# Optimization experiments

Hardware: AMD Instinct MI355X
Metric: run time of the kernel (lower is better)

Reference implementation:

```python
import jax, jax.numpy as jnp
import numpy as np

T, N = 20, 192
D_EMB, D_H, D_REL = 32, 64, 32
D_TMP = D_REL + 2 * D_H  # 160 = rel_emb + h_self + h_neighbor


def setup_inputs() -> dict:
    key = jax.random.key(0)
    ks = jax.random.split(key, 16)
    g = lambda i, shape, s: jax.random.normal(ks[i], shape, jnp.float32) * s
    inp = {
        "nodes_abs": g(0, (T, N, 2), 1.0),
        "nodes_norm": g(1, (T, N, 2), 1.0),
        "shift_value": g(2, (T, N, 2), 1.0),
        # parameters (inputLayer, LSTMCell, 2 GCNs, outputLayer)
        "w_in": g(3, (D_EMB, 2), 0.2),
        "b_in": jnp.zeros((D_EMB,), jnp.float32),
        "w_ih": g(4, (4 * D_H, D_EMB), 0.1),
        "w_hh": g(5, (4 * D_H, D_H), 0.001),
        "b_ih": jnp.zeros((4 * D_H,), jnp.float32).at[D_H:2 * D_H].set(1.0),
        "b_hh": jnp.zeros((4 * D_H,), jnp.float32),
        "w_rel": g(6, (2, D_REL, 2), 0.1),
        "b_rel": jnp.zeros((2, D_REL), jnp.float32),
        "w_gate": g(7, (2, D_H, D_TMP), 0.1),
        "b_gate": jnp.zeros((2, D_H), jnp.float32),
        "w_ar": g(8, (2, D_TMP), 0.1),
        "b_ar": jnp.zeros((2,), jnp.float32),
        "w_nei": g(9, (2, D_H, D_H), 0.1),
        "w_out": g(10, (2, D_H), 0.1),
        "b_out": jnp.zeros((2,), jnp.float32),
        # int inputs
        "seq_list": jax.random.randint(ks[11], (T, N), 0, 2).astype(jnp.int32),
        "nei_list": jax.random.randint(ks[12], (T, N, N), 0, 2).astype(jnp.int32),
        "nei_num": jax.random.randint(ks[13], (T, N), 0, N).astype(jnp.int32),
    }
    return inp


def reference(nodes_abs, nodes_norm, shift_value, w_in, b_in, w_ih, w_hh, b_ih, b_hh,
              w_rel, b_rel, w_gate, b_gate, w_ar, b_ar, w_nei, w_out, b_out,
              seq_list, nei_list, nei_num):
    eps = 1e-6

    def gcn(p, corr, nei_f, h, c, o):
        # corr: (N,N,2) relative positions pos_i - pos_j; nei_f: (N,N) 0/1 mask
        r = jax.nn.relu(jnp.einsum('ijd,rd->ijr', corr, w_rel[p]) + b_rel[p])
        tmp = jnp.concatenate([r,
                               jnp.broadcast_to(h[:, None, :], (N, N, D_H)),
                               jnp.broadcast_to(h[None, :, :], (N, N, D_H))], axis=-1)
        gate = jax.nn.sigmoid(jnp.einsum('ijt,ht->ijh', tmp, w_gate[p]) + b_gate[p])
        score = jnp.einsum('ijt,t->ij', tmp, w_ar[p]) + b_ar[p]
        score = jnp.where(nei_f > 0, score, -1e9)
        pos = jax.nn.softmax(score, axis=1) * nei_f  # masked attention over neighbors j
        msg = jnp.einsum('ij,ijh,jh->ih', pos, gate, h)  # gated, attended aggregation
        c_new = c + msg @ w_nei[p].T
        h_new = o * jnp.tanh(c_new)
        v1 = jnp.sum(gate * nei_f[:, :, None]) / (jnp.sum(nei_f) * D_H + eps)
        v2 = jnp.sum(jnp.max(pos, axis=1)) / (jnp.sum(jnp.max(nei_f, axis=1)) + eps)
        v3 = jnp.sum(nei_f) / jnp.float32(N)
        return h_new, c_new, (v1, v2, v3)

    def step(carry, xs):
        h, c, v1s, v2s, v3s = carry
        abs_t, norm_t, seq_t, nei_t = xs
        m = seq_t > 0
        mf = m.astype(jnp.float32)
        nei_f = (nei_t > 0).astype(jnp.float32) * mf[:, None] * mf[None, :]
        corr = abs_t[:, None, :] - abs_t[None, :, :]  # corr_index[i,j] = pos_i - pos_j
        x = jax.nn.relu(norm_t @ w_in.T + b_in)  # dropout is identity in eval
        gates = x @ w_ih.T + b_ih + h @ w_hh.T + b_hh
        i_g, f_g, g_g, o_g = jnp.split(gates, 4, axis=-1)
        i_g = jax.nn.sigmoid(i_g); f_g = jax.nn.sigmoid(f_g); o_g = jax.nn.sigmoid(o_g)
        c1 = f_g * c + i_g * jnp.tanh(g_g)
        h1 = o_g * jnp.tanh(c1)
        h1, c1, look = gcn(0, corr, nei_f, h1, c1, o_g)
        h1, c1, _ = gcn(1, corr, nei_f, h1, c1, o_g)
        out_t = (h1 @ w_out.T + b_out) * mf[:, None]
        h = jnp.where(m[:, None], h1, h)  # only active nodes update state
        c = jnp.where(m[:, None], c1, c)
        return (h, c, v1s + look[0], v2s + look[1], v3s + look[2]), out_t

    h0 = jnp.zeros((N, D_H), jnp.float32)
    c0 = jnp.zeros((N, D_H), jnp.float32)
    z = jnp.float32(0.0)
    xs = (nodes_abs[:-1], nodes_norm[:-1], seq_list[:-1], nei_list[:-1])
    (h, c, v1, v2, v3), outs = jax.lax.scan(step, (h0, c0, z, z, z), xs)
    outputs = jnp.concatenate([outs, jnp.zeros((1, N, 2), jnp.float32)], axis=0)
    return outputs, h, c, (v1 / T, v2 / T, v3 / T)
```

## Files before the change

### kernel.cpp

```cpp
#include <hip/hip_runtime.h>
#include <hip/hip_bf16.h>

#define T_STEPS 20
#define NSTEP   19
#define NN      192
#define DH      64
#define DE      32

enum : int {
  O_H     = 0,
  O_C     = O_H    + NN*DH,
  O_UH0   = O_C    + NN*DH,
  O_UH1   = O_UH0  + 2*NN*DH,
  O_CW    = O_UH1  + 2*NN*DH,
  O_OG    = O_CW   + NN*DH,
  O_U1    = O_OG   + NN*DH,
  O_S1    = O_U1   + NN*DH,
  O_S20   = O_S1   + NN,
  O_S21   = O_S20  + NN,
  O_ACC   = O_S21  + NN,
  O_WIHT  = O_ACC  + NSTEP*4 + 4,
  O_WHHT  = O_WIHT + 8192,
  O_BIH   = O_WHHT + 16384,
  O_WIN   = O_BIH  + 256,
  O_BIN   = O_WIN  + 64,
  O_WRELF = O_BIN  + 32,
  O_BRELF = O_WRELF+ 128,
  O_WGR   = O_BRELF+ 64,
  O_WGH1T = O_WGR  + 4096,
  O_WGH2T = O_WGH1T+ 8192,
  O_BGATE = O_WGH2T+ 8192,
  O_WARR  = O_BGATE+ 128,
  O_WARH1 = O_WARR + 64,
  O_WARH2 = O_WARH1+ 128,
  O_BAR   = O_WARH2+ 128,
  O_WNEIT = O_BAR  + 4,
  O_WOUT  = O_WNEIT+ 8192,
  O_BOUT  = O_WOUT + 128,
  O_ISF   = O_BOUT + 2,
  O_TOTAL = O_ISF  + 1
};

typedef unsigned long long ull;

__device__ __forceinline__ float bf2f(__hip_bfloat16 v) { return __bfloat162float(v); }
__device__ __forceinline__ float sigm(float x) { return 1.0f / (1.0f + __expf(-x)); }
__device__ __forceinline__ float tanh_fast(float x) {
  float e = __expf(-2.0f * fabsf(x));
  float r = (1.0f - e) / (1.0f + e);
  return copysignf(r, x);
}

__device__ __forceinline__ float ldf(const void* p, int idx, int isf32) {
  if (isf32) return ((const float*)p)[idx];
  return bf2f(((const __hip_bfloat16*)p)[idx]);
}
__device__ __forceinline__ void stf(void* p, int idx, float v, int isf32) {
  if (isf32) ((float*)p)[idx] = v;
  else       ((__hip_bfloat16*)p)[idx] = __float2bfloat16(v);
}

__device__ __forceinline__ int read_isf(const float* F, int tid, int* s_isf) {
  if (tid == 0) *s_isf = (int)F[O_ISF];
  __syncthreads();
  return *s_isf;
}

__device__ __forceinline__ void lstm_prep_dev(
    float* __restrict__ F, const void* __restrict__ nnorm, int isf32,
    int t, int i, int tid, int wave, int lane, int load_hc,
    float* s_x, float* s_hc, float* s_cc, float* s_gates, float* s_h1)
{
  if (load_hc && wave == 0) { s_hc[lane] = F[O_H + i*DH + lane]; s_cc[lane] = F[O_C + i*DH + lane]; }
  if (wave == 1 && lane < DE) {
    float nx = ldf(nnorm, (t*NN + i)*2 + 0, isf32);
    float ny = ldf(nnorm, (t*NN + i)*2 + 1, isf32);
    s_x[lane] = fmaxf(nx*F[O_WIN + lane*2] + ny*F[O_WIN + lane*2 + 1] + F[O_BIN + lane], 0.f);
  }
  __syncthreads();
  {
    int G = tid;
    float acc = F[O_BIH + G];
    for (int e = 0; e < DE; e++) acc += F[O_WIHT + e*256 + G] * s_x[e];
    for (int k = 0; k < DH; k++) acc += F[O_WHHT + k*256 + G] * s_hc[k];
    s_gates[G] = acc;
  }
  __syncthreads();
  if (wave == 0) {
    float ig = sigm(s_gates[lane]);
    float fg = sigm(s_gates[64 + lane]);
    float gg = tanh_fast(s_gates[128 + lane]);
    float og = sigm(s_gates[192 + lane]);
    float c1 = fg * s_cc[lane] + ig * gg;
    float h1 = og * tanh_fast(c1);
    int idx = i*DH + lane;
    F[O_CW  + idx] = c1;
    F[O_UH0 + 2*idx + 1] = h1;
    F[O_OG  + idx] = og;
    s_h1[lane] = h1;
  }
  __syncthreads();
  {
    int idx = i*DH + lane;
    if (wave == 0) {
      float a = 0.f;
      const float* w = F + O_WGH1T + lane;
      for (int k = 0; k < DH; k++) a += w[k*DH] * s_h1[k];
      F[O_U1 + idx] = a;
    } else if (wave == 1) {
      float a = 0.f;
      const float* w = F + O_WGH2T + lane;
      for (int k = 0; k < DH; k++) a += w[k*DH] * s_h1[k];
      F[O_UH0 + 2*idx] = a;
    } else if (wave == 2) {
      float hp = s_h1[lane];
      float a1 = hp * F[O_WARH1 + lane];
      float a2 = hp * F[O_WARH2 + lane];
      for (int o = 32; o >= 1; o >>= 1) { a1 += __shfl_xor(a1, o, 64); a2 += __shfl_xor(a2, o, 64); }
      if (lane == 0) { F[O_S1 + i] = a1; F[O_S20 + i] = a2; }
    }
  }
}

__global__ __launch_bounds__(256) void k_init(float* __restrict__ F,
                       void* __restrict__ out,
                       const void* w_in,  const void* b_in,
                       const void* w_ih,  const void* w_hh,
                       const void* b_ih,  const void* b_hh,
                       const void* w_rel, const void* b_rel,
                       const void* w_gate,const void* b_gate,
                       const void* w_ar,  const void* b_ar,
                       const void* w_nei, const void* w_out,
                       const void* b_out) {
  __shared__ int s_isf;
  const int wave = threadIdx.x >> 6, lane = threadIdx.x & 63;
  if (wave == 0) {
    const unsigned short* u = (const unsigned short*)w_gate;
    int bad = 0;
    for (int x = lane; x < 1024; x += 64) {
      float v = __uint_as_float(((unsigned)u[x]) << 16);
      if (!(fabsf(v) <= 4.0f)) bad++;
    }
    for (int o = 32; o >= 1; o >>= 1) bad += __shfl_xor(bad, o, 64);
    if (lane == 0) s_isf = (bad > 64);
  }
  __syncthreads();
  const int isf32 = s_isf;
  if (blockIdx.x == 0 && threadIdx.x == 0) F[O_ISF] = (float)isf32;

  int tid = blockIdx.x * blockDim.x + threadIdx.x;
  int stride = gridDim.x * blockDim.x;
  for (int x = tid; x < O_WIHT; x += stride) F[x] = 0.f;
  for (int x = tid; x < NN*2;  x += stride) stf(out, (T_STEPS-1)*NN*2 + x, 0.f, isf32);
  for (int x = tid; x < 8192;  x += stride) { int e = x >> 8, G = x & 255; F[O_WIHT + x] = ldf(w_ih, G*32 + e, isf32); }
  for (int x = tid; x < 16384; x += stride) { int k = x >> 8, G = x & 255; F[O_WHHT + x] = ldf(w_hh, G*64 + k, isf32); }
  for (int x = tid; x < 256;   x += stride) F[O_BIH + x] = ldf(b_ih, x, isf32) + ldf(b_hh, x, isf32);
  for (int x = tid; x < 64;    x += stride) F[O_WIN + x] = ldf(w_in, x, isf32);
  for (int x = tid; x < 32;    x += stride) F[O_BIN + x] = ldf(b_in, x, isf32);
  for (int x = tid; x < 128;   x += stride) F[O_WRELF + x] = ldf(w_rel, x, isf32);
  for (int x = tid; x < 64;    x += stride) F[O_BRELF + x] = ldf(b_rel, x, isf32);
  for (int x = tid; x < 4096;  x += stride) { int p = x >> 11, h = (x >> 5) & 63, d = x & 31;
    F[O_WGR + x] = ldf(w_gate, p*10240 + h*160 + d, isf32); }
  for (int x = tid; x < 8192;  x += stride) { int p = x >> 12, k = (x >> 6) & 63, h = x & 63;
    F[O_WGH1T + x] = ldf(w_gate, p*10240 + h*160 + 32 + k, isf32); }
  for (int x = tid; x < 8192;  x += stride) { int p = x >> 12, k = (x >> 6) & 63, h = x & 63;
    F[O_WGH2T + x] = ldf(w_gate, p*10240 + h*160 + 96 + k, isf32); }
  for (int x = tid; x < 128;   x += stride) F[O_BGATE + x] = ldf(b_gate, x, isf32);
  for (int x = tid; x < 64;    x += stride) { int p = x >> 5, d = x & 31; F[O_WARR + x] = ldf(w_ar, p*160 + d, isf32); }
  for (int x = tid; x < 128;   x += stride) { int p = x >> 6, k = x & 63; F[O_WARH1 + x] = ldf(w_ar, p*160 + 32 + k, isf32); }
  for (int x = tid; x < 128;   x += stride) { int p = x >> 6, k = x & 63; F[O_WARH2 + x] = ldf(w_ar, p*160 + 96 + k, isf32); }
  for (int x = tid; x < 2;     x += stride) F[O_BAR + x] = ldf(b_ar, x, isf32);
  for (int x = tid; x < 8192;  x += stride) { int p = x >> 12, k = (x >> 6) & 63, h = x & 63;
    F[O_WNEIT + x] = ldf(w_nei, p*4096 + h*64 + k, isf32); }
  for (int x = tid; x < 128;   x += stride) F[O_WOUT + x] = ldf(w_out, x, isf32);
  for (int x = tid; x < 2;     x += stride) F[O_BOUT + x] = ldf(b_out, x, isf32);
}

__global__ __launch_bounds__(256) void k_lstm0(float* __restrict__ F,
                                               const void* __restrict__ nnorm) {
  __shared__ float s_x[DE], s_hc[DH], s_cc[DH], s_gates[4*DH], s_h1[DH];
  __shared__ int s_isf;
  const int tid = threadIdx.x, wave = tid >> 6, lane = tid & 63;
  const int isf32 = read_isf(F, tid, &s_isf);
  lstm_prep_dev(F, nnorm, isf32, 0, blockIdx.x, tid, wave, lane, 1,
                s_x, s_hc, s_cc, s_gates, s_h1);
}

__global__ __launch_bounds__(256) void k_gcn(float* __restrict__ F,
                                             const void* __restrict__ nabs,
                                             const void* __restrict__ nnorm,
                                             const int* __restrict__ seq,
                                             const int* __restrict__ nei,
                                             void* __restrict__ out,
                                             int t, int p, int last) {
  __shared__ float s_rt[NN*33];
  __shared__ float s_score[NN], s_pos[NN], s_neif[NN];
  __shared__ int   s_jlist[NN];
  __shared__ float s_red[4*DH], s_v1[4], s_msg[DH], s_hprep[DH];
  __shared__ float s_x[DE], s_hc[DH], s_cc[DH], s_gates[4*DH], s_h1[DH];
  __shared__ int   s_isf, s_nv;

  const int tid = threadIdx.x, wave = tid >> 6, lane = tid & 63;
  const int i = blockIdx.x;
  const int isf32 = read_isf(F, tid, &s_isf);
  const int m_i = seq[t*NN + i] > 0;
  const int UHr = p ? O_UH1 : O_UH0;
  const int S2r = p ? O_S21 : O_S20;

  if (wave < 3) {
    int j  = wave*64 + lane;
    int nf = m_i && (seq[t*NN + j] > 0) && (nei[(t*NN + i)*NN + j] > 0);
    s_neif[j] = nf ? 1.f : 0.f;
    float sc = 0.f;
    if (nf) {
      float cx = ldf(nabs, (t*NN + i)*2 + 0, isf32) - ldf(nabs, (t*NN + j)*2 + 0, isf32);
      float cy = ldf(nabs, (t*NN + i)*2 + 1, isf32) - ldf(nabs, (t*NN + j)*2 + 1, isf32);
      const float* wr = F + O_WRELF + p*64;
      const float* br = F + O_BRELF + p*32;
      const float* wa = F + O_WARR  + p*32;
      float dot = 0.f;
      for (int d = 0; d < 32; d++) {
        float rv = fmaxf(cx*wr[2*d] + cy*wr[2*d+1] + br[d], 0.f);
        s_rt[j*33 + d] = rv;
        dot += rv * wa[d];
      }
      sc = dot + F[O_S1 + i] + F[S2r + j] + F[O_BAR + p];
    }
    s_score[j] = sc;
  }
  __syncthreads();

  if (wave == 0) {
    float n0 = s_neif[lane], n1 = s_neif[64+lane], n2 = s_neif[128+lane];
    float sc0 = s_score[lane], sc1 = s_score[64+lane], sc2 = s_score[128+lane];
    const float NEG = -3.0e38f;
    float mx = fmaxf(fmaxf(n0 > 0.f ? sc0 : NEG, n1 > 0.f ? sc1 : NEG),
                     n2 > 0.f ? sc2 : NEG);
    for (int o = 32; o >= 1; o >>= 1) mx = fmaxf(mx, __shfl_xor(mx, o, 64));
    float e0 = (n0 > 0.f) ? __expf(sc0 - mx) : 0.f;
    float e1 = (n1 > 0.f) ? __expf(sc1 - mx) : 0.f;
    float e2 = (n2 > 0.f) ? __expf(sc2 - mx) : 0.f;
    float s = e0 + e1 + e2;
    for (int o = 32; o >= 1; o >>= 1) s += __shfl_xor(s, o, 64);
    float inv = (s > 0.f) ? 1.0f / s : 0.f;
    float p0 = e0*inv, p1 = e1*inv, p2 = e2*inv;
    s_pos[lane] = p0; s_pos[64+lane] = p1; s_pos[128+lane] = p2;
    ull m0 = __ballot(n0 > 0.f), m1 = __ballot(n1 > 0.f), m2 = __ballot(n2 > 0.f);
    ull lt = (1ull << lane) - 1ull;
    int c0 = __popcll(m0), c1 = __popcll(m1);
    if (n0 > 0.f) s_jlist[__popcll(m0 & lt)] = lane;
    if (n1 > 0.f) s_jlist[c0 + __popcll(m1 & lt)] = 64 + lane;
    if (n2 > 0.f) s_jlist[c0 + c1 + __popcll(m2 & lt)] = 128 + lane;
    if (lane == 0) s_nv = c0 + c1 + __popcll(m2);
    if (p == 0 && m_i) {
      float cnt = n0 + n1 + n2;
      float pm  = fmaxf(fmaxf(p0, p1), p2);
      for (int o = 32; o >= 1; o >>= 1) {
        cnt += __shfl_xor(cnt, o, 64);
        pm   = fmaxf(pm, __shfl_xor(pm, o, 64));
      }
      if (lane == 0 && cnt > 0.f) {
        atomicAdd(&F[O_ACC + t*4 + 1], cnt);
        atomicAdd(&F[O_ACC + t*4 + 2], pm);
        atomicAdd(&F[O_ACC + t*4 + 3], 1.f);
      }
    }
  }
  __syncthreads();

  {
    float msg = 0.f, v1 = 0.f;
    const int nv = s_nv;
    if (m_i && nv > 0) {
      float wreg[32];
      const float* wgp = F + O_WGR + p*2048 + lane*32;
#pragma unroll
      for (int d = 0; d < 32; d++) wreg[d] = wgp[d];
      float basev = F[O_U1 + i*DH + lane] + F[O_BGATE + p*DH + lane];
      const float2* UH2 = (const float2*)(F + UHr);
      int k = wave;
      int jn = (k < nv) ? s_jlist[k] : 0;
      float2 uhn = (k < nv) ? UH2[jn*DH + lane] : make_float2(0.f, 0.f);
      for (; k < nv; k += 4) {
        int j = jn;
        float2 uh = uhn;
        int kn = k + 4;
        if (kn < nv) { jn = s_jlist[kn]; uhn = UH2[jn*DH + lane]; }
        float acc = basev + uh.x;
        const float* rr = &s_rt[j*33];
#pragma unroll
        for (int d = 0; d < 32; d++) acc += rr[d] * wreg[d];
        float g = sigm(acc);
        v1 += g;
        msg += s_pos[j] * g * uh.y;
      }
    }
    s_red[wave*DH + lane] = msg;
    for (int o = 32; o >= 1; o >>= 1) v1 += __shfl_xor(v1, o, 64);
    if (lane == 0) s_v1[wave] = v1;
  }
  __syncthreads();

  if (wave == 0) {
    s_msg[lane] = s_red[lane] + s_red[64+lane] + s_red[128+lane] + s_red[192+lane];
    if (p == 0 && m_i && lane == 0) {
      float v1t = s_v1[0] + s_v1[1] + s_v1[2] + s_v1[3];
      atomicAdd(&F[O_ACC + t*4 + 0], v1t);
    }
  }
  __syncthreads();

  if (wave == 0) {
    int idx = i*DH + lane;
    float hcom, ccom = 0.f;
    if (m_i) {
      float cn = F[O_CW + idx];
      const float* wn = F + O_WNEIT + p*4096 + lane;
      for (int k = 0; k < DH; k++) cn += s_msg[k] * wn[k*DH];
      hcom = F[O_OG + idx] * tanh_fast(cn);
      F[O_CW + idx] = cn;
      ccom = cn;
      if (p == 1) { F[O_H + idx] = hcom; F[O_C + idx] = ccom; }
    } else {
      hcom = F[UHr + 2*idx + 1];
    }
    if (p == 0) F[O_UH1 + 2*idx + 1] = hcom;
    s_hprep[lane] = hcom;
    if (p == 1) {
      s_hc[lane] = m_i ? hcom : F[O_H + idx];
      s_cc[lane] = m_i ? ccom : F[O_C + idx];
    }
  }
  __syncthreads();

  if (p == 0) {
    int idx = i*DH + lane;
    if (wave == 0) {
      float a = 0.f;
      const float* w = F + O_WGH1T + 4096 + lane;
      for (int k = 0; k < DH; k++) a += w[k*DH] * s_hprep[k];
      F[O_U1 + idx] = a;
    } else if (wave == 1) {
      float a = 0.f;
      const float* w = F + O_WGH2T + 4096 + lane;
      for (int k = 0; k < DH; k++) a += w[k*DH] * s_hprep[k];
      F[O_UH1 + 2*idx] = a;
    } else if (wave == 2) {
      float hp = s_hprep[lane];
      float a1 = hp * F[O_WARH1 + DH + lane];
      float a2 = hp * F[O_WARH2 + DH + lane];
      for (int o = 32; o >= 1; o >>= 1) { a1 += __shfl_xor(a1, o, 64); a2 += __shfl_xor(a2, o, 64); }
      if (lane == 0) { F[O_S1 + i] = a1; F[O_S21 + i] = a2; }
    }
  } else {
    if (wave == 0 && lane < 2) {
      float a = 0.f;
      if (m_i) {
        a = F[O_BOUT + lane];
        const float* wo = F + O_WOUT + lane*DH;
        for (int h = 0; h < DH; h++) a += s_hprep[h] * wo[h];
      }
      stf(out, (t*NN + i)*2 + lane, a, isf32);
    }
    if (!last) {
      lstm_prep_dev(F, nnorm, isf32, t + 1, i, tid, wave, lane, 0,
                    s_x, s_hc, s_cc, s_gates, s_h1);
    } else {
      if (wave == 0) stf(out, T_STEPS*NN*2 + i*DH + lane,         s_hc[lane], isf32);
      if (wave == 1) stf(out, T_STEPS*NN*2 + NN*DH + i*DH + lane, s_cc[lane], isf32);
      if (i == 0 && tid == 0) {
        float v1 = 0.f, v2 = 0.f, v3 = 0.f;
        for (int tt = 0; tt < NSTEP; tt++) {
          float sg = F[O_ACC + tt*4 + 0], sn = F[O_ACC + tt*4 + 1];
          float sp = F[O_ACC + tt*4 + 2], sm = F[O_ACC + tt*4 + 3];
          v1 += sg / (sn * 64.f + 1e-6f);
          v2 += sp / (sm + 1e-6f);
          v3 += sn / 192.f;
        }
        int base = T_STEPS*NN*2 + 2*NN*DH;
        stf(out, base + 0, v1 / 20.f, isf32);
        stf(out, base + 1, v2 / 20.f, isf32);
        stf(out, base + 2, v3 / 20.f, isf32);
      }
    }
  }
}

extern "C" void kernel_launch(void* const* d_in, const int* in_sizes, int n_in,
                              void* d_out, int out_size, void* d_ws, size_t ws_size,
                              hipStream_t stream) {
  const void* nabs  = d_in[0];
  const void* nnorm = d_in[1];
  const int* seq = (const int*)d_in[18];
  const int* nei = (const int*)d_in[19];
  float* F = (float*)d_ws;

  k_init<<<NN, 256, 0, stream>>>(F, d_out,
      d_in[3], d_in[4], d_in[5], d_in[6], d_in[7], d_in[8], d_in[9], d_in[10],
      d_in[11], d_in[12], d_in[13], d_in[14], d_in[15], d_in[16], d_in[17]);
  k_lstm0<<<NN, 256, 0, stream>>>(F, nnorm);
  for (int t = 0; t < NSTEP; t++) {
    k_gcn<<<NN, 256, 0, stream>>>(F, nabs, nnorm, seq, nei, d_out, t, 0, 0);
    k_gcn<<<NN, 256, 0, stream>>>(F, nabs, nnorm, seq, nei, d_out, t, 1, t == NSTEP - 1);
  }
}
```

Before: 650.7 us.

## Fuse all timesteps into one persistent kernel with software grid barrier

Replaces the 38 per-phase k_gcn launches plus k_lstm0 with a single persistent kernel (one block per node) that steps through all timesteps and both GCN phases, synchronising with a flag-based grid barrier using coherent loads and stores. LSTM weights are held in registers across steps, and per-phase intermediates go to double-indexed global buffers so there are no read/write races between phases. This targets launch overhead and the re-reading of weights, at the cost of spin-wait barriers, a reliance on all 192 blocks being co-resident, and a larger workspace (with a fallback to the old path if the workspace is too small).

```diff
diff --git a/kernel.cpp b/kernel.cpp
--- a/kernel.cpp
+++ b/kernel.cpp
@@ -19,7 +19,9 @@
   O_S20   = O_S1   + NN,
   O_S21   = O_S20  + NN,
   O_ACC   = O_S21  + NN,
-  O_WIHT  = O_ACC  + NSTEP*4 + 4,
+  O_FLAGA = O_ACC  + NSTEP*4,
+  O_FLAGR = O_FLAGA+ NN*16,
+  O_WIHT  = O_FLAGR+ NN*16,
   O_WHHT  = O_WIHT + 8192,
   O_BIH   = O_WHHT + 16384,
   O_WIN   = O_BIH  + 256,
@@ -38,7 +40,10 @@
   O_WOUT  = O_WNEIT+ 8192,
   O_BOUT  = O_WOUT + 128,
   O_ISF   = O_BOUT + 2,
-  O_TOTAL = O_ISF  + 1
+  O_WEND  = O_ISF  + 1,
+  O_UHB   = O_WEND,
+  O_S2B   = O_UHB + 2*NSTEP*2*NN*DH,
+  O_PTOT  = O_S2B + 2*NSTEP*NN
 };
 
 typedef unsigned long long ull;
@@ -66,60 +71,42 @@
   return *s_isf;
 }
 
-__device__ __forceinline__ void lstm_prep_dev(
-    float* __restrict__ F, const void* __restrict__ nnorm, int isf32,
-    int t, int i, int tid, int wave, int lane, int load_hc,
-    float* s_x, float* s_hc, float* s_cc, float* s_gates, float* s_h1)
-{
-  if (load_hc && wave == 0) { s_hc[lane] = F[O_H + i*DH + lane]; s_cc[lane] = F[O_C + i*DH + lane]; }
-  if (wave == 1 && lane < DE) {
-    float nx = ldf(nnorm, (t*NN + i)*2 + 0, isf32);
-    float ny = ldf(nnorm, (t*NN + i)*2 + 1, isf32);
-    s_x[lane] = fmaxf(nx*F[O_WIN + lane*2] + ny*F[O_WIN + lane*2 + 1] + F[O_BIN + lane], 0.f);
-  }
-  __syncthreads();
-  {
-    int G = tid;
-    float acc = F[O_BIH + G];
-    for (int e = 0; e < DE; e++) acc += F[O_WIHT + e*256 + G] * s_x[e];
-    for (int k = 0; k < DH; k++) acc += F[O_WHHT + k*256 + G] * s_hc[k];
-    s_gates[G] = acc;
-  }
-  __syncthreads();
-  if (wave == 0) {
-    float ig = sigm(s_gates[lane]);
-    float fg = sigm(s_gates[64 + lane]);
-    float gg = tanh_fast(s_gates[128 + lane]);
-    float og = sigm(s_gates[192 + lane]);
-    float c1 = fg * s_cc[lane] + ig * gg;
-    float h1 = og * tanh_fast(c1);
-    int idx = i*DH + lane;
-    F[O_CW  + idx] = c1;
-    F[O_UH0 + 2*idx + 1] = h1;
-    F[O_OG  + idx] = og;
-    s_h1[lane] = h1;
-  }
-  __syncthreads();
-  {
-    int idx = i*DH + lane;
-    if (wave == 0) {
-      float a = 0.f;
-      const float* w = F + O_WGH1T + lane;
-      for (int k = 0; k < DH; k++) a += w[k*DH] * s_h1[k];
-      F[O_U1 + idx] = a;
-    } else if (wave == 1) {
-      float a = 0.f;
-      const float* w = F + O_WGH2T + lane;
-      for (int k = 0; k < DH; k++) a += w[k*DH] * s_h1[k];
-      F[O_UH0 + 2*idx] = a;
-    } else if (wave == 2) {
-      float hp = s_h1[lane];
-      float a1 = hp * F[O_WARH1 + lane];
-      float a2 = hp * F[O_WARH2 + lane];
-      for (int o = 32; o >= 1; o >>= 1) { a1 += __shfl_xor(a1, o, 64); a2 += __shfl_xor(a2, o, 64); }
-      if (lane == 0) { F[O_S1 + i] = a1; F[O_S20 + i] = a2; }
-    }
-  }
+__device__ __forceinline__ float ld_coh_f32(const void* p) {
+  float v;
+  asm volatile("global_load_dword %0, %1, off sc0 sc1\n\ts_waitcnt vmcnt(0)"
+               : "=v"(v) : "v"(p) : "memory");
+  return v;
+}
+__device__ __forceinline__ unsigned ld_coh_u32(const void* p) {
+  unsigned v;
+  asm volatile("global_load_dword %0, %1, off sc0 sc1\n\ts_waitcnt vmcnt(0)"
+               : "=v"(v) : "v"(p) : "memory");
+  return v;
+}
+__device__ __forceinline__ void st_coh_f32(void* p, float v) {
+  asm volatile("global_store_dword %0, %1, off sc0 sc1" :: "v"(p), "v"(v) : "memory");
+}
+__device__ __forceinline__ void st_coh_u32(void* p, unsigned v) {
+  asm volatile("global_store_dword %0, %1, off sc0 sc1" :: "v"(p), "v"(v) : "memory");
+}
+
+__device__ __forceinline__ void gridbar(float* F, unsigned ep, int i, int tid) {
+  asm volatile("s_waitcnt vmcnt(0)" ::: "memory");
+  __syncthreads();
+  unsigned* flagA = (unsigned*)(F + O_FLAGA);
+  unsigned* flagR = (unsigned*)(F + O_FLAGR);
+  const unsigned tgt = ep + 1u;
+  if (tid == 0) st_coh_u32(flagA + i*16, tgt);
+  if (i == 0) {
+    if (tid < NN) {
+      while (ld_coh_u32(flagA + tid*16) < tgt) __builtin_amdgcn_s_sleep(2);
+    }
+    __syncthreads();
+    if (tid < NN) st_coh_u32(flagR + tid*16, tgt);
+  } else if (tid == 0) {
+    while (ld_coh_u32(flagR + i*16) < tgt) __builtin_amdgcn_s_sleep(1);
+  }
+  __syncthreads();
 }
 
 __global__ __launch_bounds__(256) void k_init(float* __restrict__ F,
@@ -174,6 +161,62 @@
     F[O_WNEIT + x] = ldf(w_nei, p*4096 + h*64 + k, isf32); }
   for (int x = tid; x < 128;   x += stride) F[O_WOUT + x] = ldf(w_out, x, isf32);
   for (int x = tid; x < 2;     x += stride) F[O_BOUT + x] = ldf(b_out, x, isf32);
+}
+
+__device__ __forceinline__ void lstm_prep_dev(
+    float* __restrict__ F, const void* __restrict__ nnorm, int isf32,
+    int t, int i, int tid, int wave, int lane, int load_hc,
+    float* s_x, float* s_hc, float* s_cc, float* s_gates, float* s_h1)
+{
+  if (load_hc && wave == 0) { s_hc[lane] = F[O_H + i*DH + lane]; s_cc[lane] = F[O_C + i*DH + lane]; }
+  if (wave == 1 && lane < DE) {
+    float nx = ldf(nnorm, (t*NN + i)*2 + 0, isf32);
+    float ny = ldf(nnorm, (t*NN + i)*2 + 1, isf32);
+    s_x[lane] = fmaxf(nx*F[O_WIN + lane*2] + ny*F[O_WIN + lane*2 + 1] + F[O_BIN + lane], 0.f);
+  }
+  __syncthreads();
+  {
+    int G = tid;
+    float acc = F[O_BIH + G];
+    for (int e = 0; e < DE; e++) acc += F[O_WIHT + e*256 + G] * s_x[e];
+    for (int k = 0; k < DH; k++) acc += F[O_WHHT + k*256 + G] * s_hc[k];
+    s_gates[G] = acc;
+  }
+  __syncthreads();
+  if (wave == 0) {
+    float ig = sigm(s_gates[lane]);
+    float fg = sigm(s_gates[64 + lane]);
+    float gg = tanh_fast(s_gates[128 + lane]);
+    float og = sigm(s_gates[192 + lane]);
+    float c1 = fg * s_cc[lane] + ig * gg;
+    float h1 = og * tanh_fast(c1);
+    int idx = i*DH + lane;
+    F[O_CW  + idx] = c1;
+    F[O_UH0 + 2*idx + 1] = h1;
+    F[O_OG  + idx] = og;
+    s_h1[lane] = h1;
+  }
+  __syncthreads();
+  {
+    int idx = i*DH + lane;
+    if (wave == 0) {
+      float a = 0.f;
+      const float* w = F + O_WGH1T + lane;
+      for (int k = 0; k < DH; k++) a += w[k*DH] * s_h1[k];
+      F[O_U1 + idx] = a;
+    } else if (wave == 1) {
+      float a = 0.f;
+      const float* w = F + O_WGH2T + lane;
+      for (int k = 0; k < DH; k++) a += w[k*DH] * s_h1[k];
+      F[O_UH0 + 2*idx] = a;
+    } else if (wave == 2) {
+      float hp = s_h1[lane];
+      float a1 = hp * F[O_WARH1 + lane];
+      float a2 = hp * F[O_WARH2 + lane];
+      for (int o = 32; o >= 1; o >>= 1) { a1 += __shfl_xor(a1, o, 64); a2 += __shfl_xor(a2, o, 64); }
+      if (lane == 0) { F[O_S1 + i] = a1; F[O_S20 + i] = a2; }
+    }
+  }
 }
 
 __global__ __launch_bounds__(256) void k_lstm0(float* __restrict__ F,
@@ -386,6 +429,299 @@
   }
 }
 
+__device__ __forceinline__ void lstm_prepP(
+    float* __restrict__ F, const void* __restrict__ nnorm, int isf32,
+    int t, int i, int tid, int wave, int lane,
+    const float* wih_r, const float* whh_r, float bih_r,
+    float* s_x, float* s_gates, float* s_hc, float* s_cc,
+    float* s_cw, float* s_og, float* s_u1, float* s_h1, float* s_s1)
+{
+  float* UHq = F + O_UHB + (2*t)*(2*NN*DH);
+  float* S2q = F + O_S2B + (2*t)*NN;
+  if (wave == 1 && lane < DE) {
+    float nx = ldf(nnorm, (t*NN + i)*2 + 0, isf32);
+    float ny = ldf(nnorm, (t*NN + i)*2 + 1, isf32);
+    s_x[lane] = fmaxf(nx*F[O_WIN + lane*2] + ny*F[O_WIN + lane*2 + 1] + F[O_BIN + lane], 0.f);
+  }
+  __syncthreads();
+  {
+    float acc = bih_r;
+#pragma unroll
+    for (int e = 0; e < DE; e++) acc += wih_r[e] * s_x[e];
+#pragma unroll
+    for (int k = 0; k < DH; k++) acc += whh_r[k] * s_hc[k];
+    s_gates[tid] = acc;
+  }
+  __syncthreads();
+  if (wave == 0) {
+    float ig = sigm(s_gates[lane]);
+    float fg = sigm(s_gates[64 + lane]);
+    float gg = tanh_fast(s_gates[128 + lane]);
+    float og = sigm(s_gates[192 + lane]);
+    float c1 = fg * s_cc[lane] + ig * gg;
+    float h1 = og * tanh_fast(c1);
+    s_cw[lane] = c1;
+    s_og[lane] = og;
+    s_h1[lane] = h1;
+    st_coh_f32(UHq + 2*(i*DH + lane) + 1, h1);
+  }
+  __syncthreads();
+  if (wave == 0) {
+    float a = 0.f;
+    const float* w = F + O_WGH1T + lane;
+    for (int k = 0; k < DH; k++) a += w[k*DH] * s_h1[k];
+    s_u1[lane] = a;
+  } else if (wave == 1) {
+    float a = 0.f;
+    const float* w = F + O_WGH2T + lane;
+    for (int k = 0; k < DH; k++) a += w[k*DH] * s_h1[k];
+    st_coh_f32(UHq + 2*(i*DH + lane), a);
+  } else if (wave == 2) {
+    float hp = s_h1[lane];
+    float a1 = hp * F[O_WARH1 + lane];
+    float a2 = hp * F[O_WARH2 + lane];
+    for (int o = 32; o >= 1; o >>= 1) { a1 += __shfl_xor(a1, o, 64); a2 += __shfl_xor(a2, o, 64); }
+    if (lane == 0) { *s_s1 = a1; st_coh_f32(S2q + i, a2); }
+  }
+}
+
+__global__ __launch_bounds__(256, 1) void k_main(float* __restrict__ F,
+    const void* __restrict__ nabs, const void* __restrict__ nnorm,
+    const int* __restrict__ seq, const int* __restrict__ nei,
+    void* __restrict__ out)
+{
+  __shared__ float s_rt[NN*33];
+  __shared__ float s_score[NN], s_pos[NN], s_neif[NN];
+  __shared__ int   s_jlist[NN];
+  __shared__ ull   s_cmask[3];
+  __shared__ float s_red[4*DH], s_v1[4], s_msg[DH], s_hprep[DH];
+  __shared__ float s_x[DE], s_gates[4*DH];
+  __shared__ float s_hc[DH], s_cc[DH], s_cw[DH], s_og[DH], s_u1[DH], s_h1[DH], s_s1;
+  __shared__ float s_fin[NSTEP*4];
+  __shared__ int   s_isf;
+
+  const int tid = threadIdx.x, wave = tid >> 6, lane = tid & 63;
+  const int i = blockIdx.x;
+  const int isf32 = read_isf(F, tid, &s_isf);
+
+  float wih_r[DE], whh_r[DH];
+  const float bih_r = F[O_BIH + tid];
+#pragma unroll
+  for (int e = 0; e < DE; e++) wih_r[e] = F[O_WIHT + e*256 + tid];
+#pragma unroll
+  for (int k = 0; k < DH; k++) whh_r[k] = F[O_WHHT + k*256 + tid];
+  if (wave == 0) { s_hc[lane] = 0.f; s_cc[lane] = 0.f; }
+  __syncthreads();
+
+  lstm_prepP(F, nnorm, isf32, 0, i, tid, wave, lane, wih_r, whh_r, bih_r,
+             s_x, s_gates, s_hc, s_cc, s_cw, s_og, s_u1, s_h1, &s_s1);
+
+  unsigned ep = 0;
+  for (int t = 0; t < NSTEP; ++t) {
+    const int m_i = seq[t*NN + i] > 0;
+    const int j = wave*64 + lane;
+
+    ull mymask = 0; int nf = 0;
+    if (wave < 3) {
+      nf = m_i && (seq[t*NN + j] > 0) && (nei[(t*NN + i)*NN + j] > 0);
+      s_neif[j] = nf ? 1.f : 0.f;
+      mymask = __ballot(nf != 0);
+      if (lane == 0) s_cmask[wave] = mymask;
+    }
+    __syncthreads();
+    const int c0 = __popcll(s_cmask[0]), c1 = __popcll(s_cmask[1]);
+    const int nv = c0 + c1 + __popcll(s_cmask[2]);
+    if (wave < 3 && nf) {
+      int base = (wave == 0) ? 0 : ((wave == 1) ? c0 : c0 + c1);
+      ull lt = (1ull << lane) - 1ull;
+      s_jlist[base + __popcll(mymask & lt)] = j;
+    }
+
+    for (int p = 0; p < 2; ++p) {
+      gridbar(F, ep++, i, tid);
+      const int lastT = (t == NSTEP - 1) && (p == 1);
+      const int qr = 2*t + p;
+      const float2* UH2 = (const float2*)(F + O_UHB + qr*(2*NN*DH));
+      const float* S2q = F + O_S2B + qr*NN;
+      float* UHn = F + O_UHB + (2*t+1)*(2*NN*DH);
+      float* S2n = F + O_S2B + (2*t+1)*NN;
+
+      if (wave < 3) {
+        float s2j = S2q[j];
+        float sc = 0.f, dot = 0.f;
+        if (nf) {
+          float cx = ldf(nabs, (t*NN + i)*2 + 0, isf32) - ldf(nabs, (t*NN + j)*2 + 0, isf32);
+          float cy = ldf(nabs, (t*NN + i)*2 + 1, isf32) - ldf(nabs, (t*NN + j)*2 + 1, isf32);
+          const float* wr = F + O_WRELF + p*64;
+          const float* br = F + O_BRELF + p*32;
+          const float* wa = F + O_WARR  + p*32;
+#pragma unroll
+          for (int d = 0; d < 32; d++) {
+            float rv = fmaxf(cx*wr[2*d] + cy*wr[2*d+1] + br[d], 0.f);
+            s_rt[j*33 + d] = rv;
+            dot += rv * wa[d];
+          }
+          sc = dot + s_s1 + s2j + F[O_BAR + p];
+        }
+        s_score[j] = sc;
+      }
+      __syncthreads();
+
+      if (wave == 0) {
+        float n0 = s_neif[lane], n1 = s_neif[64+lane], n2 = s_neif[128+lane];
+        float sc0 = s_score[lane], sc1 = s_score[64+lane], sc2 = s_score[128+lane];
+        const float NEG = -3.0e38f;
+        float mx = fmaxf(fmaxf(n0 > 0.f ? sc0 : NEG, n1 > 0.f ? sc1 : NEG),
+                         n2 > 0.f ? sc2 : NEG);
+        for (int o = 32; o >= 1; o >>= 1) mx = fmaxf(mx, __shfl_xor(mx, o, 64));
+        float e0 = (n0 > 0.f) ? __expf(sc0 - mx) : 0.f;
+        float e1 = (n1 > 0.f) ? __expf(sc1 - mx) : 0.f;
+        float e2 = (n2 > 0.f) ? __expf(sc2 - mx) : 0.f;
+        float s = e0 + e1 + e2;
+        for (int o = 32; o >= 1; o >>= 1) s += __shfl_xor(s, o, 64);
+        float inv = (s > 0.f) ? 1.0f / s : 0.f;
+        float p0 = e0*inv, p1 = e1*inv, p2 = e2*inv;
+        s_pos[lane] = p0; s_pos[64+lane] = p1; s_pos[128+lane] = p2;
+        if (p == 0 && m_i) {
+          float cnt = n0 + n1 + n2;
+          float pm  = fmaxf(fmaxf(p0, p1), p2);
+          for (int o = 32; o >= 1; o >>= 1) {
+            cnt += __shfl_xor(cnt, o, 64);
+            pm   = fmaxf(pm, __shfl_xor(pm, o, 64));
+          }
+          if (lane == 0 && cnt > 0.f) {
+            atomicAdd(&F[O_ACC + t*4 + 1], cnt);
+            atomicAdd(&F[O_ACC + t*4 + 2], pm);
+            atomicAdd(&F[O_ACC + t*4 + 3], 1.f);
+          }
+        }
+      }
+      __syncthreads();
+
+      {
+        float msg = 0.f, v1 = 0.f;
+        if (m_i && nv > 0) {
+          float wreg[32];
+          const float* wgp = F + O_WGR + p*2048 + lane*32;
+#pragma unroll
+          for (int d = 0; d < 32; d++) wreg[d] = wgp[d];
+          float basev = s_u1[lane] + F[O_BGATE + p*DH + lane];
+          for (int c = 0; c < 6; ++c) {
+            int k0 = wave + c*32;
+            if (k0 >= nv) break;
+            int jv[8]; float2 u[8];
+#pragma unroll
+            for (int m = 0; m < 8; m++) {
+              int kk = k0 + 4*m;
+              jv[m] = (kk < nv) ? s_jlist[kk] : 0;
+              u[m] = UH2[jv[m]*DH + lane];
+            }
+#pragma unroll
+            for (int m = 0; m < 8; m++) {
+              int kk = k0 + 4*m;
+              if (kk < nv) {
+                float acc = basev + u[m].x;
+                const float* rr = &s_rt[jv[m]*33];
+#pragma unroll
+                for (int d = 0; d < 32; d++) acc += rr[d] * wreg[d];
+                float g = sigm(acc);
+                v1 += g;
+                msg += s_pos[jv[m]] * g * u[m].y;
+              }
+            }
+          }
+        }
+        s_red[wave*DH + lane] = msg;
+        for (int o = 32; o >= 1; o >>= 1) v1 += __shfl_xor(v1, o, 64);
+        if (lane == 0) s_v1[wave] = v1;
+      }
+      __syncthreads();
+
+      if (wave == 0) {
+        s_msg[lane] = s_red[lane] + s_red[64+lane] + s_red[128+lane] + s_red[192+lane];
+        if (p == 0 && m_i && lane == 0) {
+          atomicAdd(&F[O_ACC + t*4 + 0], s_v1[0] + s_v1[1] + s_v1[2] + s_v1[3]);
+        }
+      }
+      __syncthreads();
+
+      if (wave == 0) {
+        float hcom, ccom = 0.f;
+        if (m_i) {
+          float cn = s_cw[lane];
+          const float* wn = F + O_WNEIT + p*4096 + lane;
+          for (int k = 0; k < DH; k++) cn += s_msg[k] * wn[k*DH];
+          hcom = s_og[lane] * tanh_fast(cn);
+          s_cw[lane] = cn;
+          ccom = cn;
+        } else {
+          hcom = p ? s_hprep[lane] : s_h1[lane];
+        }
+        if (p == 0) st_coh_f32(UHn + 2*(i*DH + lane) + 1, hcom);
+        s_hprep[lane] = hcom;
+        if (p == 1 && m_i) { s_hc[lane] = hcom; s_cc[lane] = ccom; }
+      }
+      __syncthreads();
+
+      if (p == 0) {
+        if (wave == 0) {
+          float a = 0.f;
+          const float* w = F + O_WGH1T + 4096 + lane;
+          for (int k = 0; k < DH; k++) a += w[k*DH] * s_hprep[k];
+          s_u1[lane] = a;
+        } else if (wave == 1) {
+          float a = 0.f;
+          const float* w = F + O_WGH2T + 4096 + lane;
+          for (int k = 0; k < DH; k++) a += w[k*DH] * s_hprep[k];
+          st_coh_f32(UHn + 2*(i*DH + lane), a);
+        } else if (wave == 2) {
+          float hp = s_hprep[lane];
+          float a1 = hp * F[O_WARH1 + DH + lane];
+          float a2 = hp * F[O_WARH2 + DH + lane];
+          for (int o = 32; o >= 1; o >>= 1) { a1 += __shfl_xor(a1, o, 64); a2 += __shfl_xor(a2, o, 64); }
+          if (lane == 0) { s_s1 = a1; st_coh_f32(S2n + i, a2); }
+        }
+      } else {
+        if (wave == 0 && lane < 2) {
+          float a = 0.f;
+          if (m_i) {
+            a = F[O_BOUT + lane];
+            const float* wo = F + O_WOUT + lane*DH;
+            for (int h = 0; h < DH; h++) a += s_hprep[h] * wo[h];
+          }
+          stf(out, (t*NN + i)*2 + lane, a, isf32);
+        }
+        if (!lastT) {
+          lstm_prepP(F, nnorm, isf32, t + 1, i, tid, wave, lane,
+                     wih_r, whh_r, bih_r,
+                     s_x, s_gates, s_hc, s_cc, s_cw, s_og, s_u1, s_h1, &s_s1);
+        } else {
+          if (wave == 0) stf(out, T_STEPS*NN*2 + i*DH + lane,         s_hc[lane], isf32);
+          if (wave == 1) stf(out, T_STEPS*NN*2 + NN*DH + i*DH + lane, s_cc[lane], isf32);
+          if (i == 0) {
+            if (tid < NSTEP*4) s_fin[tid] = ld_coh_f32(F + O_ACC + tid);
+            __syncthreads();
+            if (tid == 0) {
+              float v1 = 0.f, v2 = 0.f, v3 = 0.f;
+              for (int tt = 0; tt < NSTEP; tt++) {
+                float sg = s_fin[tt*4 + 0], sn = s_fin[tt*4 + 1];
+                float sp = s_fin[tt*4 + 2], sm = s_fin[tt*4 + 3];
+                v1 += sg / (sn * 64.f + 1e-6f);
+                v2 += sp / (sm + 1e-6f);
+                v3 += sn / 192.f;
+              }
+              int base = T_STEPS*NN*2 + 2*NN*DH;
+              stf(out, base + 0, v1 / 20.f, isf32);
+              stf(out, base + 1, v2 / 20.f, isf32);
+              stf(out, base + 2, v3 / 20.f, isf32);
+            }
+          }
+        }
+      }
+    }
+  }
+}
+
 extern "C" void kernel_launch(void* const* d_in, const int* in_sizes, int n_in,
                               void* d_out, int out_size, void* d_ws, size_t ws_size,
                               hipStream_t stream) {
@@ -398,9 +734,14 @@
   k_init<<<NN, 256, 0, stream>>>(F, d_out,
       d_in[3], d_in[4], d_in[5], d_in[6], d_in[7], d_in[8], d_in[9], d_in[10],
       d_in[11], d_in[12], d_in[13], d_in[14], d_in[15], d_in[16], d_in[17]);
-  k_lstm0<<<NN, 256, 0, stream>>>(F, nnorm);
-  for (int t = 0; t < NSTEP; t++) {
-    k_gcn<<<NN, 256, 0, stream>>>(F, nabs, nnorm, seq, nei, d_out, t, 0, 0);
-    k_gcn<<<NN, 256, 0, stream>>>(F, nabs, nnorm, seq, nei, d_out, t, 1, t == NSTEP - 1);
-  }
-}
+
+  if (ws_size >= (size_t)O_PTOT * sizeof(float)) {
+    k_main<<<NN, 256, 0, stream>>>(F, nabs, nnorm, seq, nei, d_out);
+  } else {
+    k_lstm0<<<NN, 256, 0, stream>>>(F, nnorm);
+    for (int t = 0; t < NSTEP; t++) {
+      k_gcn<<<NN, 256, 0, stream>>>(F, nabs, nnorm, seq, nei, d_out, t, 0, 0);
+      k_gcn<<<NN, 256, 0, stream>>>(F, nabs, nnorm, seq, nei, d_out, t, 1, t == NSTEP - 1);
+    }
+  }
+}
```

Result: slower. 1.222 ms (+87.8%).

## Pack four nodes per 1024-thread block and pass dtype flag from host

Applied to the files above, without the earlier changes.

Each k_gcn and k_lstm0 block now handles four graph nodes in 256-thread groups, so the grid shrinks from 192 blocks to 48 blocks of 1024 threads, with shared arrays indexed per group. The dtype flag is inferred on the host from input byte sizes and passed as a kernel argument, which removes the per-block global read and barrier used to fetch it. The aim is lower per-launch and per-block overhead across the 38 serial launches. In exchange, only 48 CUs are occupied, syncthreads span the whole 1024-thread block, and shared memory per block is roughly four times larger.

```diff
diff --git a/kernel.cpp b/kernel.cpp
--- a/kernel.cpp
+++ b/kernel.cpp
@@ -6,6 +6,8 @@
 #define NN      192
 #define DH      64
 #define DE      32
+#define RPB     4
+#define GRID    48
 
 enum : int {
   O_H     = 0,
@@ -60,15 +62,13 @@
   else       ((__hip_bfloat16*)p)[idx] = __float2bfloat16(v);
 }
 
-__device__ __forceinline__ int read_isf(const float* F, int tid, int* s_isf) {
-  if (tid == 0) *s_isf = (int)F[O_ISF];
-  __syncthreads();
-  return *s_isf;
+__device__ __forceinline__ int resolve_isf(const float* F, int isf_arg) {
+  return (isf_arg >= 0) ? isf_arg : (int)F[O_ISF];
 }
 
 __device__ __forceinline__ void lstm_prep_dev(
     float* __restrict__ F, const void* __restrict__ nnorm, int isf32,
-    int t, int i, int tid, int wave, int lane, int load_hc,
+    int t, int i, int l, int wave, int lane, int load_hc,
     float* s_x, float* s_hc, float* s_cc, float* s_gates, float* s_h1)
 {
   if (load_hc && wave == 0) { s_hc[lane] = F[O_H + i*DH + lane]; s_cc[lane] = F[O_C + i*DH + lane]; }
@@ -79,7 +79,7 @@
   }
   __syncthreads();
   {
-    int G = tid;
+    int G = l;
     float acc = F[O_BIH + G];
     for (int e = 0; e < DE; e++) acc += F[O_WIHT + e*256 + G] * s_x[e];
     for (int k = 0; k < DH; k++) acc += F[O_WHHT + k*256 + G] * s_hc[k];
@@ -131,10 +131,12 @@
                        const void* w_gate,const void* b_gate,
                        const void* w_ar,  const void* b_ar,
                        const void* w_nei, const void* w_out,
-                       const void* b_out) {
+                       const void* b_out, int isf_arg) {
   __shared__ int s_isf;
   const int wave = threadIdx.x >> 6, lane = threadIdx.x & 63;
-  if (wave == 0) {
+  if (isf_arg >= 0) {
+    if (threadIdx.x == 0) s_isf = isf_arg;
+  } else if (wave == 0) {
     const unsigned short* u = (const unsigned short*)w_gate;
     int bad = 0;
     for (int x = lane; x < 1024; x += 64) {
@@ -176,33 +178,38 @@
   for (int x = tid; x < 2;     x += stride) F[O_BOUT + x] = ldf(b_out, x, isf32);
 }
 
-__global__ __launch_bounds__(256) void k_lstm0(float* __restrict__ F,
-                                               const void* __restrict__ nnorm) {
-  __shared__ float s_x[DE], s_hc[DH], s_cc[DH], s_gates[4*DH], s_h1[DH];
-  __shared__ int s_isf;
-  const int tid = threadIdx.x, wave = tid >> 6, lane = tid & 63;
-  const int isf32 = read_isf(F, tid, &s_isf);
-  lstm_prep_dev(F, nnorm, isf32, 0, blockIdx.x, tid, wave, lane, 1,
-                s_x, s_hc, s_cc, s_gates, s_h1);
-}
-
-__global__ __launch_bounds__(256) void k_gcn(float* __restrict__ F,
-                                             const void* __restrict__ nabs,
-                                             const void* __restrict__ nnorm,
-                                             const int* __restrict__ seq,
-                                             const int* __restrict__ nei,
-                                             void* __restrict__ out,
-                                             int t, int p, int last) {
-  __shared__ float s_rt[NN*33];
-  __shared__ float s_score[NN], s_pos[NN], s_neif[NN];
-  __shared__ int   s_jlist[NN];
-  __shared__ float s_red[4*DH], s_v1[4], s_msg[DH], s_hprep[DH];
-  __shared__ float s_x[DE], s_hc[DH], s_cc[DH], s_gates[4*DH], s_h1[DH];
-  __shared__ int   s_isf, s_nv;
-
-  const int tid = threadIdx.x, wave = tid >> 6, lane = tid & 63;
-  const int i = blockIdx.x;
-  const int isf32 = read_isf(F, tid, &s_isf);
+__global__ __launch_bounds__(1024) void k_lstm0(float* __restrict__ F,
+                                                const void* __restrict__ nnorm,
+                                                int isf_arg) {
+  __shared__ float s_x[RPB][DE], s_hc[RPB][DH], s_cc[RPB][DH];
+  __shared__ float s_gates[RPB][4*DH], s_h1[RPB][DH];
+  const int tid = threadIdx.x, rg = tid >> 8, l = tid & 255;
+  const int wave = l >> 6, lane = l & 63;
+  const int isf32 = resolve_isf(F, isf_arg);
+  lstm_prep_dev(F, nnorm, isf32, 0, blockIdx.x*RPB + rg, l, wave, lane, 1,
+                s_x[rg], s_hc[rg], s_cc[rg], s_gates[rg], s_h1[rg]);
+}
+
+__global__ __launch_bounds__(1024) void k_gcn(float* __restrict__ F,
+                                              const void* __restrict__ nabs,
+                                              const void* __restrict__ nnorm,
+                                              const int* __restrict__ seq,
+                                              const int* __restrict__ nei,
+                                              void* __restrict__ out,
+                                              int t, int p, int last,
+                                              int isf_arg) {
+  __shared__ float s_rt[RPB][NN*33];
+  __shared__ float s_score[RPB][NN], s_pos[RPB][NN], s_neif[RPB][NN];
+  __shared__ int   s_jlist[RPB][NN];
+  __shared__ float s_red[RPB][4*DH], s_v1[RPB][4], s_msg[RPB][DH], s_hprep[RPB][DH];
+  __shared__ float s_x[RPB][DE], s_hc[RPB][DH], s_cc[RPB][DH];
+  __shared__ float s_gates[RPB][4*DH], s_h1[RPB][DH];
+  __shared__ int   s_nv[RPB];
+
+  const int tid = threadIdx.x, rg = tid >> 8, l = tid & 255;
+  const int wave = l >> 6, lane = l & 63;
+  const int i = blockIdx.x*RPB + rg;
+  const int isf32 = resolve_isf(F, isf_arg);
   const int m_i = seq[t*NN + i] > 0;
   const int UHr = p ? O_UH1 : O_UH0;
   const int S2r = p ? O_S21 : O_S20;
@@ -210,7 +217,7 @@
   if (wave < 3) {
     int j  = wave*64 + lane;
     int nf = m_i && (seq[t*NN + j] > 0) && (nei[(t*NN + i)*NN + j] > 0);
-    s_neif[j] = nf ? 1.f : 0.f;
+    s_neif[rg][j] = nf ? 1.f : 0.f;
     float sc = 0.f;
     if (nf) {
       float cx = ldf(nabs, (t*NN + i)*2 + 0, isf32) - ldf(nabs, (t*NN + j)*2 + 0, isf32);
@@ -221,18 +228,18 @@
       float dot = 0.f;
       for (int d = 0; d < 32; d++) {
         float rv = fmaxf(cx*wr[2*d] + cy*wr[2*d+1] + br[d], 0.f);
-        s_rt[j*33 + d] = rv;
+        s_rt[rg][j*33 + d] = rv;
         dot += rv * wa[d];
       }
       sc = dot + F[O_S1 + i] + F[S2r + j] + F[O_BAR + p];
     }
-    s_score[j] = sc;
+    s_score[rg][j] = sc;
   }
   __syncthreads();
 
   if (wave == 0) {
-    float n0 = s_neif[lane], n1 = s_neif[64+lane], n2 = s_neif[128+lane];
-    float sc0 = s_score[lane], sc1 = s_score[64+lane], sc2 = s_score[128+lane];
+    float n0 = s_neif[rg][lane], n1 = s_neif[rg][64+lane], n2 = s_neif[rg][128+lane];
+    float sc0 = s_score[rg][lane], sc1 = s_score[rg][64+lane], sc2 = s_score[rg][128+lane];
     const float NEG = -3.0e38f;
     float mx = fmaxf(fmaxf(n0 > 0.f ? sc0 : NEG, n1 > 0.f ? sc1 : NEG),
                      n2 > 0.f ? sc2 : NEG);
@@ -244,14 +251,14 @@
     for (int o = 32; o >= 1; o >>= 1) s += __shfl_xor(s, o, 64);
     float inv = (s > 0.f) ? 1.0f / s : 0.f;
     float p0 = e0*inv, p1 = e1*inv, p2 = e2*inv;
-    s_pos[lane] = p0; s_pos[64+lane] = p1; s_pos[128+lane] = p2;
+    s_pos[rg][lane] = p0; s_pos[rg][64+lane] = p1; s_pos[rg][128+lane] = p2;
     ull m0 = __ballot(n0 > 0.f), m1 = __ballot(n1 > 0.f), m2 = __ballot(n2 > 0.f);
     ull lt = (1ull << lane) - 1ull;
     int c0 = __popcll(m0), c1 = __popcll(m1);
-    if (n0 > 0.f) s_jlist[__popcll(m0 & lt)] = lane;
-    if (n1 > 0.f) s_jlist[c0 + __popcll(m1 & lt)] = 64 + lane;
-    if (n2 > 0.f) s_jlist[c0 + c1 + __popcll(m2 & lt)] = 128 + lane;
-    if (lane == 0) s_nv = c0 + c1 + __popcll(m2);
+    if (n0 > 0.f) s_jlist[rg][__popcll(m0 & lt)] = lane;
+    if (n1 > 0.f) s_jlist[rg][c0 + __popcll(m1 & lt)] = 64 + lane;
+    if (n2 > 0.f) s_jlist[rg][c0 + c1 + __popcll(m2 & lt)] = 128 + lane;
+    if (lane == 0) s_nv[rg] = c0 + c1 + __popcll(m2);
     if (p == 0 && m_i) {
       float cnt = n0 + n1 + n2;
       float pm  = fmaxf(fmaxf(p0, p1), p2);
@@ -270,7 +277,7 @@
 
   {
     float msg = 0.f, v1 = 0.f;
-    const int nv = s_nv;
+    const int nv = s_nv[rg];
     if (m_i && nv > 0) {
       float wreg[32];
       const float* wgp = F + O_WGR + p*2048 + lane*32;
@@ -279,32 +286,33 @@
       float basev = F[O_U1 + i*DH + lane] + F[O_BGATE + p*DH + lane];
       const float2* UH2 = (const float2*)(F + UHr);
       int k = wave;
-      int jn = (k < nv) ? s_jlist[k] : 0;
+      int jn = (k < nv) ? s_jlist[rg][k] : 0;
       float2 uhn = (k < nv) ? UH2[jn*DH + lane] : make_float2(0.f, 0.f);
       for (; k < nv; k += 4) {
         int j = jn;
         float2 uh = uhn;
         int kn = k + 4;
-        if (kn < nv) { jn = s_jlist[kn]; uhn = UH2[jn*DH + lane]; }
+        if (kn < nv) { jn = s_jlist[rg][kn]; uhn = UH2[jn*DH + lane]; }
         float acc = basev + uh.x;
-        const float* rr = &s_rt[j*33];
+        const float* rr = &s_rt[rg][j*33];
 #pragma unroll
         for (int d = 0; d < 32; d++) acc += rr[d] * wreg[d];
         float g = sigm(acc);
         v1 += g;
-        msg += s_pos[j] * g * uh.y;
-      }
-    }
-    s_red[wave*DH + lane] = msg;
+        msg += s_pos[rg][j] * g * uh.y;
+      }
+    }
+    s_red[rg][wave*DH + lane] = msg;
     for (int o = 32; o >= 1; o >>= 1) v1 += __shfl_xor(v1, o, 64);
-    if (lane == 0) s_v1[wave] = v1;
+    if (lane == 0) s_v1[rg][wave] = v1;
   }
   __syncthreads();
 
   if (wave == 0) {
-    s_msg[lane] = s_red[lane] + s_red[64+lane] + s_red[128+lane] + s_red[192+lane];
+    s_msg[rg][lane] = s_red[rg][lane] + s_red[rg][64+lane]
+                    + s_red[rg][128+lane] + s_red[rg][192+lane];
     if (p == 0 && m_i && lane == 0) {
-      float v1t = s_v1[0] + s_v1[1] + s_v1[2] + s_v1[3];
+      float v1t = s_v1[rg][0] + s_v1[rg][1] + s_v1[rg][2] + s_v1[rg][3];
       atomicAdd(&F[O_ACC + t*4 + 0], v1t);
     }
   }
@@ -316,7 +324,7 @@
     if (m_i) {
       float cn = F[O_CW + idx];
       const float* wn = F + O_WNEIT + p*4096 + lane;
-      for (int k = 0; k < DH; k++) cn += s_msg[k] * wn[k*DH];
+      for (int k = 0; k < DH; k++) cn += s_msg[rg][k] * wn[k*DH];
       hcom = F[O_OG + idx] * tanh_fast(cn);
       F[O_CW + idx] = cn;
       ccom = cn;
@@ -325,10 +333,10 @@
       hcom = F[UHr + 2*idx + 1];
     }
     if (p == 0) F[O_UH1 + 2*idx + 1] = hcom;
-    s_hprep[lane] = hcom;
+    s_hprep[rg][lane] = hcom;
     if (p == 1) {
-      s_hc[lane] = m_i ? hcom : F[O_H + idx];
-      s_cc[lane] = m_i ? ccom : F[O_C + idx];
+      s_hc[rg][lane] = m_i ? hcom : F[O_H + idx];
+      s_cc[rg][lane] = m_i ? ccom : F[O_C + idx];
     }
   }
   __syncthreads();
@@ -338,15 +346,15 @@
     if (wave == 0) {
       float a = 0.f;
       const float* w = F + O_WGH1T + 4096 + lane;
-      for (int k = 0; k < DH; k++) a += w[k*DH] * s_hprep[k];
+      for (int k = 0; k < DH; k++) a += w[k*DH] * s_hprep[rg][k];
       F[O_U1 + idx] = a;
     } else if (wave == 1) {
       float a = 0.f;
       const float* w = F + O_WGH2T + 4096 + lane;
-      for (int k = 0; k < DH; k++) a += w[k*DH] * s_hprep[k];
+      for (int k = 0; k < DH; k++) a += w[k*DH] * s_hprep[rg][k];
       F[O_UH1 + 2*idx] = a;
     } else if (wave == 2) {
-      float hp = s_hprep[lane];
+      float hp = s_hprep[rg][lane];
       float a1 = hp * F[O_WARH1 + DH + lane];
       float a2 = hp * F[O_WARH2 + DH + lane];
       for (int o = 32; o >= 1; o >>= 1) { a1 += __shfl_xor(a1, o, 64); a2 += __shfl_xor(a2, o, 64); }
@@ -358,17 +366,17 @@
       if (m_i) {
         a = F[O_BOUT + lane];
         const float* wo = F + O_WOUT + lane*DH;
-        for (int h = 0; h < DH; h++) a += s_hprep[h] * wo[h];
+        for (int h = 0; h < DH; h++) a += s_hprep[rg][h] * wo[h];
       }
       stf(out, (t*NN + i)*2 + lane, a, isf32);
     }
     if (!last) {
-      lstm_prep_dev(F, nnorm, isf32, t + 1, i, tid, wave, lane, 0,
-                    s_x, s_hc, s_cc, s_gates, s_h1);
+      lstm_prep_dev(F, nnorm, isf32, t + 1, i, l, wave, lane, 0,
+                    s_x[rg], s_hc[rg], s_cc[rg], s_gates[rg], s_h1[rg]);
     } else {
-      if (wave == 0) stf(out, T_STEPS*NN*2 + i*DH + lane,         s_hc[lane], isf32);
-      if (wave == 1) stf(out, T_STEPS*NN*2 + NN*DH + i*DH + lane, s_cc[lane], isf32);
-      if (i == 0 && tid == 0) {
+      if (wave == 0) stf(out, T_STEPS*NN*2 + i*DH + lane,         s_hc[rg][lane], isf32);
+      if (wave == 1) stf(out, T_STEPS*NN*2 + NN*DH + i*DH + lane, s_cc[rg][lane], isf32);
+      if (blockIdx.x == 0 && tid == 0) {
         float v1 = 0.f, v2 = 0.f, v3 = 0.f;
         for (int tt = 0; tt < NSTEP; tt++) {
           float sg = F[O_ACC + tt*4 + 0], sn = F[O_ACC + tt*4 + 1];
@@ -395,12 +403,18 @@
   const int* nei = (const int*)d_in[19];
   float* F = (float*)d_ws;
 
+  int isf = -1;
+  if (n_in > 11 && in_sizes) {
+    if      (in_sizes[11] == 81920) isf = 1;
+    else if (in_sizes[11] == 40960) isf = 0;
+  }
+
   k_init<<<NN, 256, 0, stream>>>(F, d_out,
       d_in[3], d_in[4], d_in[5], d_in[6], d_in[7], d_in[8], d_in[9], d_in[10],
-      d_in[11], d_in[12], d_in[13], d_in[14], d_in[15], d_in[16], d_in[17]);
-  k_lstm0<<<NN, 256, 0, stream>>>(F, nnorm);
+      d_in[11], d_in[12], d_in[13], d_in[14], d_in[15], d_in[16], d_in[17], isf);
+  k_lstm0<<<GRID, 1024, 0, stream>>>(F, nnorm, isf);
   for (int t = 0; t < NSTEP; t++) {
-    k_gcn<<<NN, 256, 0, stream>>>(F, nabs, nnorm, seq, nei, d_out, t, 0, 0);
-    k_gcn<<<NN, 256, 0, stream>>>(F, nabs, nnorm, seq, nei, d_out, t, 1, t == NSTEP - 1);
-  }
-}
+    k_gcn<<<GRID, 1024, 0, stream>>>(F, nabs, nnorm, seq, nei, d_out, t, 0, 0, isf);
+    k_gcn<<<GRID, 1024, 0, stream>>>(F, nabs, nnorm, seq, nei, d_out, t, 1, t == NSTEP - 1, isf);
+  }
+}
```

Result: slower. 931.9 us (+43.2%).
